# Kernel optimization log

Hardware: AMD Instinct MI355X
Metric: run time of the kernel (lower is better)

## Reference

```python
import jax, jax.numpy as jnp
import numpy as np

N = 100000       # nodes
E = 1200000      # edges
D_IN = 64
D_OUT = 64
ALPHA = 0.01     # LeakyReLU negative slope
EPS = 1e-5       # BatchNorm eps


def setup_inputs() -> dict:
    key = jax.random.key(0)
    k0, k1, k2, k3 = jax.random.split(key, 4)
    x = jax.random.normal(k0, (N, D_IN), dtype=jnp.float32)
    edge_idx = jax.random.randint(k1, (2, E), 0, N)
    edge_attr = jax.random.uniform(k2, (E,), dtype=jnp.float32)
    W = jax.random.normal(k3, (D_IN, D_OUT), dtype=jnp.float32) * (1.0 / np.sqrt(D_IN))
    b = jnp.zeros((D_OUT,), dtype=jnp.float32)
    gamma = jnp.ones((D_OUT,), dtype=jnp.float32)
    beta = jnp.zeros((D_OUT,), dtype=jnp.float32)
    return {"x": x, "edge_idx": edge_idx, "edge_attr": edge_attr,
            "W": W, "b": b, "gamma": gamma, "beta": beta}


def reference(x, edge_idx, edge_attr, W, b, gamma, beta):
    n = x.shape[0]
    row, col = edge_idx[0], edge_idx[1]
    # --- GCNConv: add self-loops, symmetric normalization ---
    loops = jnp.arange(n)
    row_f = jnp.concatenate([row, loops])                       # [E+N]
    col_f = jnp.concatenate([col, loops])                       # [E+N]
    w_f = jnp.concatenate([edge_attr, jnp.ones((n,), x.dtype)])  # [E+N]
    deg = jax.ops.segment_sum(w_f, col_f, num_segments=n)       # [N]
    deg_safe = jnp.where(deg > 0, deg, 1.0)
    dis = jnp.where(deg > 0, jax.lax.rsqrt(deg_safe), 0.0)      # deg^-1/2
    norm = dis[row_f] * w_f * dis[col_f]                        # [E+N]
    h = x @ W                                                   # [N, D_OUT]
    msg = norm[:, None] * h[row_f]                              # gather + scale
    agg = jax.ops.segment_sum(msg, col_f, num_segments=n) + b   # scatter-add
    # --- BatchNorm (training-mode batch stats, biased var) ---
    mean = jnp.mean(agg, axis=0)
    var = jnp.mean((agg - mean) ** 2, axis=0)
    hn = (agg - mean) * jax.lax.rsqrt(var + EPS) * gamma + beta
    # --- LeakyReLU ---
    return jnp.where(hn >= 0, hn, ALPHA * hn)
```

## Files before the change

### kernel.cpp

```cpp
#include <hip/hip_runtime.h>

#define D 64
#define ALPHA 0.01f
#define EPS 1e-5f
#define NREP 8
#define CAP 48
#define GSZ 128
#define GMAX 1024
#define NB 512
#define CHUNK 2368
#define BT 512
#define WTP 72
#define GEMM_BLOCKS 512

typedef __attribute__((ext_vector_type(8))) short short8;
typedef __attribute__((ext_vector_type(4))) float f32x4;

__device__ inline unsigned short f2bf(float f) {
    unsigned u = __float_as_uint(f);
    u += 0x7fffu + ((u >> 16) & 1u);
    return (unsigned short)(u >> 16);
}
__device__ inline float bf2f(unsigned short h) { return __uint_as_float((unsigned)h << 16); }

__global__ __launch_bounds__(BT) void k_prepbin(const float4* __restrict__ x4,
                                                ushort4* __restrict__ xb4,
                                                float* __restrict__ stats,
                                                const int* __restrict__ eidx,
                                                const float* __restrict__ w,
                                                uint2* __restrict__ seg,
                                                unsigned short* __restrict__ off16,
                                                long long n16, int G, int E, int chunk) {
    __shared__ uint2 rec[CHUNK];
    __shared__ int h[GMAX + 2];
    __shared__ int ls[BT];
    if (blockIdx.x < NB) {
        int b = blockIdx.x, t = threadIdx.x;
        int e0 = b * chunk;
        int e1 = e0 + chunk; if (e1 > E) e1 = E;
        for (int i = t; i < GMAX + 2; i += BT) h[i] = 0;
        __syncthreads();
        for (int e = e0 + t; e < e1; e += BT) {
            int row = eidx[e];
            int c = eidx[E + e];
            unsigned wq = (unsigned)(w[e] * 32767.0f + 0.5f);
            rec[e - e0] = make_uint2((wq << 17) | (unsigned)row, (unsigned)c);
            atomicAdd(&h[c >> 7], 1);
        }
        __syncthreads();
        int i0 = 2 * t, i1 = 2 * t + 1;
        int a0 = h[i0];
        int a1 = h[i1];
        ls[t] = a0 + a1;
        __syncthreads();
        int own = ls[t];
        for (int off = 1; off < BT; off <<= 1) {
            int v = (t >= off) ? ls[t - off] : 0;
            __syncthreads();
            ls[t] += v;
            __syncthreads();
        }
        int excl = ls[t] - own;
        __syncthreads();
        h[i0] = excl;
        h[i1] = excl + a0;
        __syncthreads();
        unsigned short* ob = off16 + (size_t)b * (G + 1);
        for (int g = t; g <= G; g += BT) ob[g] = (unsigned short)h[g];
        __syncthreads();
        for (int e = e0 + t; e < e1; e += BT) {
            uint2 rv = rec[e - e0];
            int c = (int)rv.y;
            int slot = atomicAdd(&h[c >> 7], 1);
            seg[e0 + slot] = make_uint2(rv.x, (unsigned)(c & (GSZ - 1)));
        }
    } else {
        long long i = (long long)(blockIdx.x - NB) * BT + threadIdx.x;
        if (i < n16) {
            float4 v = x4[i];
            ushort4 r;
            r.x = f2bf(v.x); r.y = f2bf(v.y); r.z = f2bf(v.z); r.w = f2bf(v.w);
            xb4[i] = r;
        }
        if (i < NREP * 128) stats[i] = 0.0f;
    }
}

__global__ __launch_bounds__(BT) void k_binC2(const uint2* __restrict__ seg,
                                              const unsigned short* __restrict__ off16,
                                              unsigned* __restrict__ bucket,
                                              int* __restrict__ cnt,
                                              float* __restrict__ dis,
                                              float* __restrict__ dis_s,
                                              int G, int chunk, int n) {
    __shared__ int cl[GSZ];
    __shared__ float ws[GSZ];
    int g = blockIdx.x;
    if (threadIdx.x < GSZ) { cl[threadIdx.x] = 0; ws[threadIdx.x] = 0.0f; }
    __syncthreads();
    int b = threadIdx.x;
    const unsigned short* ob = off16 + (size_t)b * (G + 1);
    int s = ob[g], e = ob[g + 1];
    size_t base = (size_t)b * chunk;
    for (int i = s; i < e; ++i) {
        uint2 ev = seg[base + i];
        int cig = (int)ev.y;
        int rank = atomicAdd(&cl[cig], 1);
        atomicAdd(&ws[cig], (float)(ev.x >> 17) * (1.0f / 32767.0f));
        int node = g * GSZ + cig;
        if (rank < CAP) bucket[(size_t)node * CAP + rank] = ev.x;
    }
    __syncthreads();
    if (threadIdx.x < GSZ) {
        int node = g * GSZ + threadIdx.x;
        if (node < n) {
            cnt[node] = cl[threadIdx.x];
            float d = rsqrtf(1.0f + ws[threadIdx.x]);
            dis[node] = d;
            dis_s[node] = d * (1.0f / 32767.0f);
        }
    }
}

__global__ __launch_bounds__(256) void k_gather(const unsigned short* __restrict__ xb,
                                                const unsigned* __restrict__ bucket,
                                                const int* __restrict__ cnt,
                                                const float* __restrict__ dis,
                                                const float* __restrict__ dis_s,
                                                unsigned short* __restrict__ aggb, int n) {
    int node = blockIdx.x * 4 + (threadIdx.x >> 6);
    if (node >= n) return;
    int lane = threadIdx.x & 63;
    int g = lane >> 3;
    int l = lane & 7;
    int c = cnt[node];
    if (c > CAP) c = CAP;
    float di = dis[node];
    float acc[8] = {0, 0, 0, 0, 0, 0, 0, 0};
    if (g == 0) {
        short8 xv = *(const short8*)(xb + ((size_t)node << 6) + l * 8);
#pragma unroll
        for (int k = 0; k < 8; ++k) acc[k] = bf2f((unsigned short)xv[k]) * di;
    }
    const unsigned* bkt = bucket + (size_t)node * CAP;
    int j0 = g, j1 = g + 8;
    unsigned v0 = (j0 < c) ? bkt[j0] : 0u;
    unsigned v1 = (j1 < c) ? bkt[j1] : 0u;
    while (j0 < c) {
        int p0 = j0 + 16, p1 = j1 + 16;
        unsigned w0 = (p0 < c) ? bkt[p0] : 0u;
        unsigned w1 = (p1 < c) ? bkt[p1] : 0u;
        int s0 = (int)(v0 & 0x1FFFFu);
        int s1 = (int)(v1 & 0x1FFFFu);
        float nr0 = (float)(v0 >> 17) * dis_s[s0];
        float nr1 = (float)(v1 >> 17) * dis_s[s1];
        short8 x0 = *(const short8*)(xb + ((size_t)s0 << 6) + l * 8);
        short8 x1 = *(const short8*)(xb + ((size_t)s1 << 6) + l * 8);
#pragma unroll
        for (int k = 0; k < 8; ++k) acc[k] += nr0 * bf2f((unsigned short)x0[k]);
#pragma unroll
        for (int k = 0; k < 8; ++k) acc[k] += nr1 * bf2f((unsigned short)x1[k]);
        v0 = w0; v1 = w1; j0 = p0; j1 = p1;
    }
#pragma unroll
    for (int off = 8; off <= 32; off <<= 1)
#pragma unroll
        for (int k = 0; k < 8; ++k) acc[k] += __shfl_xor(acc[k], off, 64);
    if (g == 0) {
        short8 r;
#pragma unroll
        for (int k = 0; k < 8; ++k) r[k] = (short)f2bf(acc[k] * di);
        *(short8*)(aggb + ((size_t)node << 6) + l * 8) = r;
    }
}

__global__ __launch_bounds__(256) void k_gemmstats(const unsigned short* __restrict__ aggb,
                                                   const float* __restrict__ Wm,
                                                   float* __restrict__ stats, int n) {
    __shared__ unsigned short Wt[64 * WTP];
    __shared__ float ssum[4][64], qsum[4][64];
    int tid = threadIdx.x;
    for (int i = tid; i < 4096; i += 256) {
        int k = i >> 6, nn = i & 63;
        Wt[nn * WTP + k] = f2bf(Wm[i]);
    }
    __syncthreads();
    int wv = tid >> 6;
    int lane = tid & 63;
    int l15 = lane & 15;
    int quad = lane >> 4;

    short8 bfrag[2][4];
#pragma unroll
    for (int h = 0; h < 2; ++h)
#pragma unroll
        for (int g = 0; g < 4; ++g)
            bfrag[h][g] = *(const short8*)&Wt[(g * 16 + l15) * WTP + h * 32 + quad * 8];

    float s[4] = {0, 0, 0, 0}, q[4] = {0, 0, 0, 0};
    int nwt = (n + 15) >> 4;
    for (int wt = blockIdx.x * 4 + wv; wt < nwt; wt += gridDim.x * 4) {
        int row0 = wt * 16;
        int arow = row0 + l15;
        if (arow >= n) arow = n - 1;
        const unsigned short* ap = aggb + (size_t)arow * 64 + quad * 8;
        short8 a0 = *(const short8*)ap;
        short8 a1 = *(const short8*)(ap + 32);
        f32x4 acc[4] = {{0, 0, 0, 0}, {0, 0, 0, 0}, {0, 0, 0, 0}, {0, 0, 0, 0}};
#pragma unroll
        for (int g = 0; g < 4; ++g) {
            acc[g] = __builtin_amdgcn_mfma_f32_16x16x32_bf16(a0, bfrag[0][g], acc[g], 0, 0, 0);
            acc[g] = __builtin_amdgcn_mfma_f32_16x16x32_bf16(a1, bfrag[1][g], acc[g], 0, 0, 0);
        }
#pragma unroll
        for (int r = 0; r < 4; ++r) {
            int row = row0 + quad * 4 + r;
            if (row < n) {
#pragma unroll
                for (int g = 0; g < 4; ++g) {
                    float v = acc[g][r];
                    s[g] += v;
                    q[g] += v * v;
                }
            }
        }
    }
#pragma unroll
    for (int off = 16; off <= 32; off <<= 1) {
#pragma unroll
        for (int g = 0; g < 4; ++g) {
            s[g] += __shfl_xor(s[g], off, 64);
            q[g] += __shfl_xor(q[g], off, 64);
        }
    }
    if (quad == 0) {
#pragma unroll
        for (int g = 0; g < 4; ++g) { ssum[wv][g * 16 + l15] = s[g]; qsum[wv][g * 16 + l15] = q[g]; }
    }
    __syncthreads();
    float* st = stats + (blockIdx.x & (NREP - 1)) * 128;
    if (tid < 64)
        atomicAdd(&st[tid], ssum[0][tid] + ssum[1][tid] + ssum[2][tid] + ssum[3][tid]);
    else if (tid < 128) {
        int t = tid - 64;
        atomicAdd(&st[64 + t], qsum[0][t] + qsum[1][t] + qsum[2][t] + qsum[3][t]);
    }
}

__global__ __launch_bounds__(256) void k_gemmbn(const unsigned short* __restrict__ aggb,
                                                const float* __restrict__ Wm,
                                                float* __restrict__ out,
                                                const float* __restrict__ stats,
                                                const float* __restrict__ gamma,
                                                const float* __restrict__ beta, int n) {
    __shared__ unsigned short Wt[64 * WTP];
    __shared__ float scale[64], shift[64];
    int tid = threadIdx.x;
    for (int i = tid; i < 4096; i += 256) {
        int k = i >> 6, nn = i & 63;
        Wt[nn * WTP + k] = f2bf(Wm[i]);
    }
    if (tid < 64) {
        float sm = 0.0f, qm = 0.0f;
#pragma unroll
        for (int r = 0; r < NREP; ++r) {
            sm += stats[r * 128 + tid];
            qm += stats[r * 128 + 64 + tid];
        }
        float inv_n = 1.0f / (float)n;
        float mean = sm * inv_n;
        float var = qm * inv_n - mean * mean;
        float sc = rsqrtf(var + EPS) * gamma[tid];
        scale[tid] = sc;
        shift[tid] = beta[tid] - mean * sc;
    }
    __syncthreads();
    int wv = tid >> 6;
    int lane = tid & 63;
    int l15 = lane & 15;
    int quad = lane >> 4;

    short8 bfrag[2][4];
    float bsc[4], bsh[4];
#pragma unroll
    for (int h = 0; h < 2; ++h)
#pragma unroll
        for (int g = 0; g < 4; ++g)
            bfrag[h][g] = *(const short8*)&Wt[(g * 16 + l15) * WTP + h * 32 + quad * 8];
#pragma unroll
    for (int g = 0; g < 4; ++g) { bsc[g] = scale[g * 16 + l15]; bsh[g] = shift[g * 16 + l15]; }

    int nwt = (n + 15) >> 4;
    for (int wt = blockIdx.x * 4 + wv; wt < nwt; wt += gridDim.x * 4) {
        int row0 = wt * 16;
        int arow = row0 + l15;
        if (arow >= n) arow = n - 1;
        const unsigned short* ap = aggb + (size_t)arow * 64 + quad * 8;
        short8 a0 = *(const short8*)ap;
        short8 a1 = *(const short8*)(ap + 32);
        f32x4 acc[4] = {{0, 0, 0, 0}, {0, 0, 0, 0}, {0, 0, 0, 0}, {0, 0, 0, 0}};
#pragma unroll
        for (int g = 0; g < 4; ++g) {
            acc[g] = __builtin_amdgcn_mfma_f32_16x16x32_bf16(a0, bfrag[0][g], acc[g], 0, 0, 0);
            acc[g] = __builtin_amdgcn_mfma_f32_16x16x32_bf16(a1, bfrag[1][g], acc[g], 0, 0, 0);
        }
#pragma unroll
        for (int r = 0; r < 4; ++r) {
            int row = row0 + quad * 4 + r;
            if (row < n) {
                size_t base = (size_t)row * 64;
#pragma unroll
                for (int g = 0; g < 4; ++g) {
                    float v = acc[g][r] * bsc[g] + bsh[g];
                    v = v >= 0.0f ? v : ALPHA * v;
                    out[base + g * 16 + l15] = v;
                }
            }
        }
    }
}

extern "C" void kernel_launch(void* const* d_in, const int* in_sizes, int n_in,
                              void* d_out, int out_size, void* d_ws, size_t ws_size,
                              hipStream_t stream) {
    const float* x     = (const float*)d_in[0];
    const int*   eidx  = (const int*)d_in[1];
    const float* eattr = (const float*)d_in[2];
    const float* Wm    = (const float*)d_in[3];
    const float* gamma = (const float*)d_in[5];
    const float* beta  = (const float*)d_in[6];
    float* out = (float*)d_out;

    int n = in_sizes[0] / D;
    int E = in_sizes[2];
    int G = (n + GSZ - 1) / GSZ;
    int chunk = (E + NB - 1) / NB;

    char* p = (char*)d_ws;
    uint2* seg = (uint2*)p;                     p += (size_t)E * 8;
    unsigned* bucket = (unsigned*)p;            p += (size_t)n * CAP * 4;
    unsigned short* xb   = (unsigned short*)p;  p += (size_t)n * D * 2;
    unsigned short* aggb = (unsigned short*)p;  p += (size_t)n * D * 2;
    int* cnt = (int*)p;                         p += (size_t)n * 4;
    float* dis = (float*)p;                     p += (size_t)n * 4;
    float* dis_s = (float*)p;                   p += (size_t)n * 4;
    float* stats = (float*)p;                   p += NREP * 128 * 4;
    unsigned short* off16 = (unsigned short*)p; p += (((size_t)NB * (G + 1) * 2 + 15) & ~15ULL);

    long long n16 = (long long)n * 16;
    unsigned prep_blocks = (unsigned)((n16 + BT - 1) / BT);

    k_prepbin<<<NB + prep_blocks, BT, 0, stream>>>(
        (const float4*)x, (ushort4*)xb, stats, eidx, eattr, seg, off16, n16, G, E, chunk);
    k_binC2<<<G, BT, 0, stream>>>(seg, off16, bucket, cnt, dis, dis_s, G, chunk, n);
    k_gather<<<(n + 3) / 4, 256, 0, stream>>>(xb, bucket, cnt, dis, dis_s, aggb, n);
    k_gemmstats<<<GEMM_BLOCKS, 256, 0, stream>>>(aggb, Wm, stats, n);
    k_gemmbn<<<GEMM_BLOCKS, 256, 0, stream>>>(aggb, Wm, out, stats, gamma, beta, n);
}
```

Measured before the change: 171.9 us.

## Fuse per-node bucketing into gather kernel using shared-memory buckets

The binning kernel no longer writes a global per-node bucket array and counts. It now only computes degree normalization. A new aggregation kernel, launched once per 128-node group, re-reads the segmented edges, builds the 128x48 bucket in LDS, and then gathers with 8 waves looping over the group's nodes. This removes the global bucket write and read traffic, at the cost of reading seg twice and launching only about 782 large blocks with 24KB+ LDS each, which may limit occupancy and latency hiding during the gather.

```diff
diff --git a/kernel.cpp b/kernel.cpp
--- a/kernel.cpp
+++ b/kernel.cpp
@@ -86,17 +86,14 @@
     }
 }
 
-__global__ __launch_bounds__(BT) void k_binC2(const uint2* __restrict__ seg,
-                                              const unsigned short* __restrict__ off16,
-                                              unsigned* __restrict__ bucket,
-                                              int* __restrict__ cnt,
-                                              float* __restrict__ dis,
-                                              float* __restrict__ dis_s,
-                                              int G, int chunk, int n) {
-    __shared__ int cl[GSZ];
+__global__ __launch_bounds__(BT) void k_disc(const uint2* __restrict__ seg,
+                                             const unsigned short* __restrict__ off16,
+                                             float* __restrict__ dis,
+                                             float* __restrict__ dis_s,
+                                             int G, int chunk, int n) {
     __shared__ float ws[GSZ];
     int g = blockIdx.x;
-    if (threadIdx.x < GSZ) { cl[threadIdx.x] = 0; ws[threadIdx.x] = 0.0f; }
+    if (threadIdx.x < GSZ) ws[threadIdx.x] = 0.0f;
     __syncthreads();
     int b = threadIdx.x;
     const unsigned short* ob = off16 + (size_t)b * (G + 1);
@@ -104,17 +101,12 @@
     size_t base = (size_t)b * chunk;
     for (int i = s; i < e; ++i) {
         uint2 ev = seg[base + i];
-        int cig = (int)ev.y;
-        int rank = atomicAdd(&cl[cig], 1);
-        atomicAdd(&ws[cig], (float)(ev.x >> 17) * (1.0f / 32767.0f));
-        int node = g * GSZ + cig;
-        if (rank < CAP) bucket[(size_t)node * CAP + rank] = ev.x;
+        atomicAdd(&ws[ev.y], (float)(ev.x >> 17) * (1.0f / 32767.0f));
     }
     __syncthreads();
     if (threadIdx.x < GSZ) {
         int node = g * GSZ + threadIdx.x;
         if (node < n) {
-            cnt[node] = cl[threadIdx.x];
             float d = rsqrtf(1.0f + ws[threadIdx.x]);
             dis[node] = d;
             dis_s[node] = d * (1.0f / 32767.0f);
@@ -122,55 +114,78 @@
     }
 }
 
-__global__ __launch_bounds__(256) void k_gather(const unsigned short* __restrict__ xb,
-                                                const unsigned* __restrict__ bucket,
-                                                const int* __restrict__ cnt,
-                                                const float* __restrict__ dis,
-                                                const float* __restrict__ dis_s,
-                                                unsigned short* __restrict__ aggb, int n) {
-    int node = blockIdx.x * 4 + (threadIdx.x >> 6);
-    if (node >= n) return;
-    int lane = threadIdx.x & 63;
-    int g = lane >> 3;
+__global__ __launch_bounds__(BT) void k_aggf(const unsigned short* __restrict__ xb,
+                                             const uint2* __restrict__ seg,
+                                             const unsigned short* __restrict__ off16,
+                                             const float* __restrict__ dis,
+                                             const float* __restrict__ dis_s,
+                                             unsigned short* __restrict__ aggb,
+                                             int G, int chunk, int n) {
+    __shared__ unsigned lbkt[GSZ * CAP];
+    __shared__ int cl[GSZ];
+    __shared__ float dl[GSZ];
+    int g = blockIdx.x, tid = threadIdx.x;
+    int base = g * GSZ;
+    if (tid < GSZ) {
+        cl[tid] = 0;
+        int node = base + tid;
+        dl[tid] = (node < n) ? dis[node] : 0.0f;
+    }
+    __syncthreads();
+    {
+        const unsigned short* ob = off16 + (size_t)tid * (G + 1);
+        int s = ob[g], e = ob[g + 1];
+        size_t sb = (size_t)tid * chunk;
+        for (int i = s; i < e; ++i) {
+            uint2 ev = seg[sb + i];
+            int cig = (int)ev.y;
+            int rank = atomicAdd(&cl[cig], 1);
+            if (rank < CAP) lbkt[cig * CAP + rank] = ev.x;
+        }
+    }
+    __syncthreads();
+    int wv = tid >> 6;
+    int lane = tid & 63;
+    int gs = lane >> 3;
     int l = lane & 7;
-    int c = cnt[node];
-    if (c > CAP) c = CAP;
-    float di = dis[node];
-    float acc[8] = {0, 0, 0, 0, 0, 0, 0, 0};
-    if (g == 0) {
-        short8 xv = *(const short8*)(xb + ((size_t)node << 6) + l * 8);
-#pragma unroll
-        for (int k = 0; k < 8; ++k) acc[k] = bf2f((unsigned short)xv[k]) * di;
-    }
-    const unsigned* bkt = bucket + (size_t)node * CAP;
-    int j0 = g, j1 = g + 8;
-    unsigned v0 = (j0 < c) ? bkt[j0] : 0u;
-    unsigned v1 = (j1 < c) ? bkt[j1] : 0u;
-    while (j0 < c) {
-        int p0 = j0 + 16, p1 = j1 + 16;
-        unsigned w0 = (p0 < c) ? bkt[p0] : 0u;
-        unsigned w1 = (p1 < c) ? bkt[p1] : 0u;
-        int s0 = (int)(v0 & 0x1FFFFu);
-        int s1 = (int)(v1 & 0x1FFFFu);
-        float nr0 = (float)(v0 >> 17) * dis_s[s0];
-        float nr1 = (float)(v1 >> 17) * dis_s[s1];
-        short8 x0 = *(const short8*)(xb + ((size_t)s0 << 6) + l * 8);
-        short8 x1 = *(const short8*)(xb + ((size_t)s1 << 6) + l * 8);
-#pragma unroll
-        for (int k = 0; k < 8; ++k) acc[k] += nr0 * bf2f((unsigned short)x0[k]);
-#pragma unroll
-        for (int k = 0; k < 8; ++k) acc[k] += nr1 * bf2f((unsigned short)x1[k]);
-        v0 = w0; v1 = w1; j0 = p0; j1 = p1;
-    }
-#pragma unroll
-    for (int off = 8; off <= 32; off <<= 1)
-#pragma unroll
-        for (int k = 0; k < 8; ++k) acc[k] += __shfl_xor(acc[k], off, 64);
-    if (g == 0) {
-        short8 r;
-#pragma unroll
-        for (int k = 0; k < 8; ++k) r[k] = (short)f2bf(acc[k] * di);
-        *(short8*)(aggb + ((size_t)node << 6) + l * 8) = r;
+    for (int ni = wv; ni < GSZ; ni += BT / 64) {
+        int node = base + ni;
+        if (node >= n) break;
+        int c = cl[ni]; if (c > CAP) c = CAP;
+        float di = dl[ni];
+        float acc[8] = {0, 0, 0, 0, 0, 0, 0, 0};
+        if (gs == 0) {
+            short8 xv = *(const short8*)(xb + ((size_t)node << 6) + l * 8);
+#pragma unroll
+            for (int k = 0; k < 8; ++k) acc[k] = bf2f((unsigned short)xv[k]) * di;
+        }
+        const unsigned* lb = lbkt + ni * CAP;
+        int j0 = gs, j1 = gs + 8;
+        while (j0 < c) {
+            unsigned v0 = lb[j0];
+            unsigned v1 = (j1 < c) ? lb[j1] : 0u;
+            int s0 = (int)(v0 & 0x1FFFFu);
+            int s1 = (int)(v1 & 0x1FFFFu);
+            float nr0 = (float)(v0 >> 17) * dis_s[s0];
+            float nr1 = (float)(v1 >> 17) * dis_s[s1];
+            short8 x0 = *(const short8*)(xb + ((size_t)s0 << 6) + l * 8);
+            short8 x1 = *(const short8*)(xb + ((size_t)s1 << 6) + l * 8);
+#pragma unroll
+            for (int k = 0; k < 8; ++k) acc[k] += nr0 * bf2f((unsigned short)x0[k]);
+#pragma unroll
+            for (int k = 0; k < 8; ++k) acc[k] += nr1 * bf2f((unsigned short)x1[k]);
+            j0 += 16; j1 += 16;
+        }
+#pragma unroll
+        for (int off = 8; off <= 32; off <<= 1)
+#pragma unroll
+            for (int k = 0; k < 8; ++k) acc[k] += __shfl_xor(acc[k], off, 64);
+        if (gs == 0) {
+            short8 r;
+#pragma unroll
+            for (int k = 0; k < 8; ++k) r[k] = (short)f2bf(acc[k] * di);
+            *(short8*)(aggb + ((size_t)node << 6) + l * 8) = r;
+        }
     }
 }
 
@@ -338,10 +353,8 @@
 
     char* p = (char*)d_ws;
     uint2* seg = (uint2*)p;                     p += (size_t)E * 8;
-    unsigned* bucket = (unsigned*)p;            p += (size_t)n * CAP * 4;
     unsigned short* xb   = (unsigned short*)p;  p += (size_t)n * D * 2;
     unsigned short* aggb = (unsigned short*)p;  p += (size_t)n * D * 2;
-    int* cnt = (int*)p;                         p += (size_t)n * 4;
     float* dis = (float*)p;                     p += (size_t)n * 4;
     float* dis_s = (float*)p;                   p += (size_t)n * 4;
     float* stats = (float*)p;                   p += NREP * 128 * 4;
@@ -352,8 +365,8 @@
 
     k_prepbin<<<NB + prep_blocks, BT, 0, stream>>>(
         (const float4*)x, (ushort4*)xb, stats, eidx, eattr, seg, off16, n16, G, E, chunk);
-    k_binC2<<<G, BT, 0, stream>>>(seg, off16, bucket, cnt, dis, dis_s, G, chunk, n);
-    k_gather<<<(n + 3) / 4, 256, 0, stream>>>(xb, bucket, cnt, dis, dis_s, aggb, n);
+    k_disc<<<G, BT, 0, stream>>>(seg, off16, dis, dis_s, G, chunk, n);
+    k_aggf<<<G, BT, 0, stream>>>(xb, seg, off16, dis, dis_s, aggb, G, chunk, n);
     k_gemmstats<<<GEMM_BLOCKS, 256, 0, stream>>>(aggb, Wm, stats, n);
     k_gemmbn<<<GEMM_BLOCKS, 256, 0, stream>>>(aggb, Wm, out, stats, gamma, beta, n);
 }
```

Result: slower. 194.8 us (+13.4%).
